# Performance work log

Hardware: AMD Instinct MI355X
Metric: run time of the kernel (lower is better)

The kernel has to match this reference:

```python
import jax, jax.numpy as jnp
import numpy as np

D_MODEL = 1024
NHEAD = 16
D_K = D_MODEL // NHEAD


def setup_inputs() -> dict:
    key = jax.random.key(0)
    ks = jax.random.split(key, 12)
    B, S = 1, 4096
    s = 1.0 / np.sqrt(D_MODEL)
    inp = {
        "query": jax.random.normal(ks[0], (B, S, D_MODEL), jnp.float32),
        "key": jax.random.normal(ks[1], (B, S, D_MODEL), jnp.float32),
        "value": jax.random.normal(ks[2], (B, S, D_MODEL), jnp.float32),
        "W_q": jax.random.normal(ks[3], (D_MODEL, D_MODEL), jnp.float32) * s,
        "b_q": jnp.zeros((D_MODEL,), jnp.float32),
        "W_k": jax.random.normal(ks[4], (D_MODEL, D_MODEL), jnp.float32) * s,
        "b_k": jnp.zeros((D_MODEL,), jnp.float32),
        "W_v": jax.random.normal(ks[5], (D_MODEL, D_MODEL), jnp.float32) * s,
        "b_v": jnp.zeros((D_MODEL,), jnp.float32),
        "W_o": jax.random.normal(ks[6], (D_MODEL, D_MODEL), jnp.float32) * s,
        "b_o": jnp.zeros((D_MODEL,), jnp.float32),
    }
    return inp


def reference(query, key, value, W_q, b_q, W_k, b_k, W_v, b_v, W_o, b_o):
    B, S, _ = query.shape
    # linear projections (torch Linear: x @ W.T + b)
    Q = query @ W_q.T + b_q
    K = key @ W_k.T + b_k
    V = value @ W_v.T + b_v
    # split heads: [B, S, D] -> [B, H, S, d_k]
    Q = Q.reshape(B, S, NHEAD, D_K).transpose(0, 2, 1, 3)
    K = K.reshape(B, S, NHEAD, D_K).transpose(0, 2, 1, 3)
    V = V.reshape(B, S, NHEAD, D_K).transpose(0, 2, 1, 3)
    # scaled dot-product attention (materializes [B,H,S,S] like original)
    scores = jnp.einsum("bhqd,bhkd->bhqk", Q, K) / jnp.sqrt(jnp.float32(D_K))
    weights = jax.nn.softmax(scores, axis=-1)
    attn = jnp.einsum("bhqk,bhkd->bhqd", weights, V)
    # combine heads: [B, H, S, d_k] -> [B, S, D]
    attn = attn.transpose(0, 2, 1, 3).reshape(B, S, D_MODEL)
    return attn @ W_o.T + b_o
```

## Files before the change

kernel.cpp:

```cpp
#include <hip/hip_runtime.h>
#include <hip/hip_bf16.h>
#include <type_traits>

constexpr int SEQ = 4096;
constexpr int DMODEL = 1024;
constexpr int NH = 16;
constexpr int DKH = 64;
constexpr float SCALE = 0.125f;
constexpr float SCALE2 = 0.125f * 1.4426950408889634f;

typedef __bf16 bf16x8 __attribute__((ext_vector_type(8)));
typedef __bf16 bf16x4 __attribute__((ext_vector_type(4)));
typedef float f32x4 __attribute__((ext_vector_type(4)));
typedef float f32x16 __attribute__((ext_vector_type(16)));
typedef unsigned int u32x4 __attribute__((ext_vector_type(4)));
union W8 { u32x4 u; bf16x8 v; };

__device__ inline void store_c(__hip_bfloat16* p, float v) { *p = __float2bfloat16(v); }
__device__ inline void store_c(float* p, float v) { *p = v; }

typedef const void __attribute__((address_space(1)))* gas_ptr;
typedef void __attribute__((address_space(3)))* las_ptr;
__device__ inline void load_lds_16B(const void* g, void* l) {
  __builtin_amdgcn_global_load_lds((gas_ptr)g, (las_ptr)l, 16, 0, 0);
}

__device__ inline unsigned pack2(float a, float b) {
  union { __bf16 h[2]; unsigned u; } p;
  p.h[0] = (__bf16)a; p.h[1] = (__bf16)b;
  return p.u;
}

__device__ inline void st8(__hip_bfloat16* buf, int row, int col, bf16x8 v) {
  *(bf16x8*)(buf + row * 64 + (col ^ ((row & 7) << 3))) = v;
}
__device__ inline bf16x8 ld8(const __hip_bfloat16* buf, int row, int col) {
  return *(const bf16x8*)(buf + row * 64 + (col ^ ((row & 7) << 3)));
}

__global__ __launch_bounds__(256)
void cvt_all(const float* __restrict__ q, const float* __restrict__ k,
             const float* __restrict__ v, const float* __restrict__ wq,
             const float* __restrict__ wk, const float* __restrict__ wv,
             const float* __restrict__ wo,
             __bf16* __restrict__ Xq, __bf16* __restrict__ Xk,
             __bf16* __restrict__ Xv, __bf16* __restrict__ Wqb,
             __bf16* __restrict__ Wkb, __bf16* __restrict__ Wvb,
             __bf16* __restrict__ Wob) {
  const int b = blockIdx.x;
  const float* src; __bf16* dst; size_t base;
  if      (b < 2048) { src = q;  dst = Xq;  base = b; }
  else if (b < 4096) { src = k;  dst = Xk;  base = b - 2048; }
  else if (b < 6144) { src = v;  dst = Xv;  base = b - 4096; }
  else if (b < 6656) { src = wq; dst = Wqb; base = b - 6144; }
  else if (b < 7168) { src = wk; dst = Wkb; base = b - 6656; }
  else if (b < 7680) { src = wv; dst = Wvb; base = b - 7168; }
  else               { src = wo; dst = Wob; base = b - 7680; }
  const size_t i = (base * 256 + threadIdx.x) * 8;
  const float4 a = *(const float4*)(src + i);
  const float4 c = *(const float4*)(src + i + 4);
  bf16x8 r = {(__bf16)a.x, (__bf16)a.y, (__bf16)a.z, (__bf16)a.w,
              (__bf16)c.x, (__bf16)c.y, (__bf16)c.z, (__bf16)c.w};
  *(bf16x8*)(dst + i) = r;
}

constexpr int BK = 64;

template <typename TC, bool TRANS_C>
__global__ __launch_bounds__(256)
void gemm_bf16_lds(const __bf16* __restrict__ A,
                   const __bf16* __restrict__ W,
                   const float* __restrict__ bias,
                   TC* __restrict__ C,
                   float out_scale) {
  __shared__ alignas(16) __bf16 As[64][64];
  __shared__ alignas(16) __bf16 Ws[64][64];

  const int t = threadIdx.x;
  const int lane = t & 63;
  const int w = t >> 6;
  const int wr = w >> 1;
  const int wc = w & 1;
  const int col = lane & 15;
  const int quad = lane >> 4;
  const int m_blk = blockIdx.y * 64;
  const int n_blk = blockIdx.x * 64;

  const int srow = t >> 3;
  const int scol = (t & 7) * 8;

  f32x4 acc[2][2] = {};

  for (int k0 = 0; k0 < DMODEL; k0 += BK) {
    __syncthreads();
    #pragma unroll
    for (int p = 0; p < 2; ++p)
      load_lds_16B(A + (size_t)(m_blk + p * 32 + srow) * DMODEL + k0 + scol,
                   &As[p * 32 + srow][scol]);
    #pragma unroll
    for (int p = 0; p < 2; ++p)
      load_lds_16B(W + (size_t)(n_blk + p * 32 + srow) * DMODEL + k0 + scol,
                   &Ws[p * 32 + srow][scol]);
    __syncthreads();

    #pragma unroll
    for (int kh = 0; kh < BK; kh += 32) {
      bf16x8 af[2], bfr[2];
      #pragma unroll
      for (int at = 0; at < 2; ++at)
        af[at] = *(const bf16x8*)&As[wr * 32 + at * 16 + col][kh + quad * 8];
      #pragma unroll
      for (int bt = 0; bt < 2; ++bt)
        bfr[bt] = *(const bf16x8*)&Ws[wc * 32 + bt * 16 + col][kh + quad * 8];
      #pragma unroll
      for (int at = 0; at < 2; ++at)
        #pragma unroll
        for (int bt = 0; bt < 2; ++bt)
          acc[at][bt] = __builtin_amdgcn_mfma_f32_16x16x32_bf16(
              af[at], bfr[bt], acc[at][bt], 0, 0, 0);
    }
  }

  #pragma unroll
  for (int at = 0; at < 2; ++at) {
    #pragma unroll
    for (int bt = 0; bt < 2; ++bt) {
      const int n = n_blk + wc * 32 + bt * 16 + col;
      const float b = bias[n];
      #pragma unroll
      for (int i = 0; i < 4; ++i) {
        const int m = m_blk + wr * 32 + at * 16 + quad * 4 + i;
        const float v = (acc[at][bt][i] + b) * out_scale;
        if constexpr (TRANS_C) store_c(&C[(size_t)n * SEQ + m], v);
        else                   store_c(&C[(size_t)m * DMODEL + n], v);
      }
    }
  }
}

constexpr int LDK = 72;

template <typename TA, typename TC, bool TRANS_C>
__global__ __launch_bounds__(256)
void gemm_tiled(const TA* __restrict__ A,
                const float* __restrict__ W,
                const float* __restrict__ bias,
                TC* __restrict__ C,
                float out_scale) {
  __shared__ alignas(16) __bf16 As[128][LDK];
  __shared__ alignas(16) __bf16 Ws[64][LDK];

  const int t = threadIdx.x;
  const int lane = t & 63;
  const int w = t >> 6;
  const int wr = w >> 1;
  const int wc = w & 1;
  const int col = lane & 15;
  const int quad = lane >> 4;
  const int m_blk = blockIdx.y * 128;
  const int n_blk = blockIdx.x * 64;

  f32x4 acc[4][2] = {};

  for (int k0 = 0; k0 < DMODEL; k0 += BK) {
    __syncthreads();
    if constexpr (std::is_same<TA, float>::value) {
      #pragma unroll
      for (int p = 0; p < 8; ++p) {
        const int r = p * 16 + (t >> 4);
        const int c = (t & 15) * 4;
        const float4 v =
            *(const float4*)(A + (size_t)(m_blk + r) * DMODEL + k0 + c);
        bf16x4 b = {(__bf16)v.x, (__bf16)v.y, (__bf16)v.z, (__bf16)v.w};
        *(bf16x4*)&As[r][c] = b;
      }
    } else {
      #pragma unroll
      for (int p = 0; p < 4; ++p) {
        const int r = p * 32 + (t >> 3);
        const int c = (t & 7) * 8;
        *(bf16x8*)&As[r][c] =
            *(const bf16x8*)((const __bf16*)A + (size_t)(m_blk + r) * DMODEL + k0 + c);
      }
    }
    #pragma unroll
    for (int p = 0; p < 4; ++p) {
      const int r = p * 16 + (t >> 4);
      const int c = (t & 15) * 4;
      const float4 v =
          *(const float4*)(W + (size_t)(n_blk + r) * DMODEL + k0 + c);
      bf16x4 b = {(__bf16)v.x, (__bf16)v.y, (__bf16)v.z, (__bf16)v.w};
      *(bf16x4*)&Ws[r][c] = b;
    }
    __syncthreads();

    #pragma unroll
    for (int kh = 0; kh < BK; kh += 32) {
      bf16x8 af[4], bfr[2];
      #pragma unroll
      for (int at = 0; at < 4; ++at)
        af[at] = *(const bf16x8*)&As[wr * 64 + at * 16 + col][kh + quad * 8];
      #pragma unroll
      for (int bt = 0; bt < 2; ++bt)
        bfr[bt] = *(const bf16x8*)&Ws[wc * 32 + bt * 16 + col][kh + quad * 8];
      #pragma unroll
      for (int at = 0; at < 4; ++at)
        #pragma unroll
        for (int bt = 0; bt < 2; ++bt)
          acc[at][bt] = __builtin_amdgcn_mfma_f32_16x16x32_bf16(
              af[at], bfr[bt], acc[at][bt], 0, 0, 0);
    }
  }

  #pragma unroll
  for (int at = 0; at < 4; ++at) {
    #pragma unroll
    for (int bt = 0; bt < 2; ++bt) {
      const int n = n_blk + wc * 32 + bt * 16 + col;
      const float b = bias[n];
      #pragma unroll
      for (int i = 0; i < 4; ++i) {
        const int m = m_blk + wr * 64 + at * 16 + quad * 4 + i;
        const float v = (acc[at][bt][i] + b) * out_scale;
        if constexpr (TRANS_C) store_c(&C[(size_t)n * SEQ + m], v);
        else                   store_c(&C[(size_t)m * DMODEL + n], v);
      }
    }
  }
}

__global__ __launch_bounds__(256, 4)
void flash_attn_split32(const __hip_bfloat16* __restrict__ Q,
                        const __hip_bfloat16* __restrict__ K,
                        const __hip_bfloat16* __restrict__ Vt,
                        __hip_bfloat16* __restrict__ Opart,
                        float* __restrict__ lsum_g) {
  __shared__ alignas(16) __hip_bfloat16 kt[64 * 64];
  __shared__ alignas(16) __hip_bfloat16 vtt[64 * 64];

  const int t = threadIdx.x;
  const int lane = t & 63;
  const int w = t >> 6;
  const int head = blockIdx.y;
  const int q0 = blockIdx.x * 128;
  const int z = blockIdx.z;
  const int l31 = lane & 31;
  const int hl = lane >> 5;

  bf16x8 qf[4];
  {
    const __hip_bfloat16* qp =
        Q + (size_t)(q0 + w * 32 + l31) * DMODEL + head * DKH + hl * 8;
    #pragma unroll
    for (int db = 0; db < 4; ++db) qf[db] = *(const bf16x8*)(qp + db * 16);
  }

  f32x16 acc_o[2] = {};
  float lsa = 0.f, lsb = 0.f;

  const int sr = t >> 2;
  const int sc = (t & 3) * 16;
  const int kbeg = z * (SEQ / 2);
  constexpr int NT = (SEQ / 2) / 64;

  const __hip_bfloat16* kgp = K + (size_t)(kbeg + sr) * DMODEL + head * DKH + sc;
  const __hip_bfloat16* vgp = Vt + (size_t)(head * DKH + sr) * SEQ + kbeg + sc;

  bf16x8 kr0 = *(const bf16x8*)kgp;
  bf16x8 kr1 = *(const bf16x8*)(kgp + 8);
  bf16x8 vr0 = *(const bf16x8*)vgp;
  bf16x8 vr1 = *(const bf16x8*)(vgp + 8);

  for (int ti = 0; ti < NT; ++ti) {
    __syncthreads();
    st8(kt, sr, sc, kr0);  st8(kt, sr, sc + 8, kr1);
    st8(vtt, sr, sc, vr0); st8(vtt, sr, sc + 8, vr1);
    __syncthreads();

    if (ti + 1 < NT) {
      const __hip_bfloat16* kn = kgp + (size_t)(ti + 1) * 64 * DMODEL;
      const __hip_bfloat16* vn = vgp + (ti + 1) * 64;
      kr0 = *(const bf16x8*)kn; kr1 = *(const bf16x8*)(kn + 8);
      vr0 = *(const bf16x8*)vn; vr1 = *(const bf16x8*)(vn + 8);
    }

    bf16x8 pa[4];
    #pragma unroll
    for (int kb = 0; kb < 2; ++kb) {
      f32x16 s = {};
      #pragma unroll
      for (int db = 0; db < 4; ++db) {
        const bf16x8 kf = ld8(kt, kb * 32 + l31, db * 16 + hl * 8);
        s = __builtin_amdgcn_mfma_f32_32x32x16_bf16(kf, qf[db], s, 0, 0, 0);
      }
      unsigned wp[8];
      #pragma unroll
      for (int i = 0; i < 8; ++i) {
        const float p0 = __builtin_amdgcn_exp2f(s[2 * i]);
        const float p1 = __builtin_amdgcn_exp2f(s[2 * i + 1]);
        lsa += p0; lsb += p1;
        wp[i] = pack2(p0, p1);
      }
      #pragma unroll
      for (int b = 0; b < 2; ++b) {
        const unsigned x0 = (unsigned)__shfl_xor((int)wp[4 * b + 0], 32);
        const unsigned x1 = (unsigned)__shfl_xor((int)wp[4 * b + 1], 32);
        const unsigned x2 = (unsigned)__shfl_xor((int)wp[4 * b + 2], 32);
        const unsigned x3 = (unsigned)__shfl_xor((int)wp[4 * b + 3], 32);
        W8 u;
        u.u[0] = hl ? x2 : wp[4 * b + 0];
        u.u[1] = hl ? x3 : wp[4 * b + 1];
        u.u[2] = hl ? wp[4 * b + 2] : x0;
        u.u[3] = hl ? wp[4 * b + 3] : x1;
        pa[kb * 2 + b] = u.v;
      }
    }

    #pragma unroll
    for (int db = 0; db < 2; ++db)
      #pragma unroll
      for (int kq = 0; kq < 4; ++kq) {
        const bf16x8 vb = ld8(vtt, db * 32 + l31, kq * 16 + hl * 8);
        acc_o[db] = __builtin_amdgcn_mfma_f32_32x32x16_bf16(
            pa[kq], vb, acc_o[db], 0, 0, 0);
      }
  }

  float lsumq = lsa + lsb;
  lsumq += __shfl_xor(lsumq, 32);
  if (lane < 32)
    lsum_g[((size_t)z * NH + head) * SEQ + q0 + w * 32 + lane] = lsumq;

  __hip_bfloat16* O = Opart + (size_t)z * SEQ * DMODEL;
  #pragma unroll
  for (int db = 0; db < 2; ++db)
    #pragma unroll
    for (int r = 0; r < 16; ++r) {
      const int qr = q0 + w * 32 + (r & 3) + 8 * (r >> 2) + 4 * hl;
      const int c = head * DKH + db * 32 + l31;
      O[(size_t)qr * DMODEL + c] = __float2bfloat16(acc_o[db][r]);
    }
}

__global__ __launch_bounds__(256)
void attn_combine(const __hip_bfloat16* __restrict__ Op,
                  const float* __restrict__ ls,
                  __hip_bfloat16* __restrict__ Ao) {
  const size_t i = ((size_t)blockIdx.x * 256 + threadIdx.x) * 8;
  const int qrow = (int)(i >> 10);
  const int h = (int)((i & 1023) >> 6);
  const float inv = 1.f / (ls[(size_t)h * SEQ + qrow] +
                           ls[(size_t)(NH + h) * SEQ + qrow]);
  const bf16x8 a = *(const bf16x8*)(Op + i);
  const bf16x8 b = *(const bf16x8*)(Op + (size_t)SEQ * DMODEL + i);
  bf16x8 r;
  #pragma unroll
  for (int j = 0; j < 8; ++j)
    r[j] = (__bf16)(((float)a[j] + (float)b[j]) * inv);
  *(bf16x8*)(Ao + i) = r;
}

constexpr int LDP = 72;
constexpr float SHIFT = 8.0f;

__global__ __launch_bounds__(256)
void flash_attn_mono(const __hip_bfloat16* __restrict__ Q,
                     const __hip_bfloat16* __restrict__ K,
                     const __hip_bfloat16* __restrict__ Vt,
                     __hip_bfloat16* __restrict__ O) {
  __shared__ alignas(16) __hip_bfloat16 kt[64][LDP];
  __shared__ alignas(16) __hip_bfloat16 vtt[DKH][LDP];
  __shared__ alignas(16) __hip_bfloat16 plT[4][32][LDP];

  const int t = threadIdx.x;
  const int lane = t & 63;
  const int w = t >> 6;
  const int h = blockIdx.y;
  const int q0 = blockIdx.x * 128;
  const int col = lane & 15;
  const int quad = lane >> 4;

  bf16x8 qf[2][2];
  #pragma unroll
  for (int rg = 0; rg < 2; ++rg) {
    const __hip_bfloat16* qptr =
        Q + (size_t)(q0 + w * 32 + rg * 16 + col) * DMODEL + h * DKH + quad * 8;
    qf[rg][0] = *(const bf16x8*)qptr;
    qf[rg][1] = *(const bf16x8*)(qptr + 32);
  }

  f32x4 acc_o[2][4] = {};
  float lsumq[2] = {0.f, 0.f};
  const int sr = t >> 2;
  const int sc = (t & 3) * 16;

  for (int k0 = 0; k0 < SEQ; k0 += 64) {
    __syncthreads();
    const __hip_bfloat16* kg = K + (size_t)(k0 + sr) * DMODEL + h * DKH + sc;
    *(bf16x8*)&kt[sr][sc]     = *(const bf16x8*)kg;
    *(bf16x8*)&kt[sr][sc + 8] = *(const bf16x8*)(kg + 8);
    const __hip_bfloat16* vg = Vt + (size_t)(h * DKH + sr) * SEQ + k0 + sc;
    *(bf16x8*)&vtt[sr][sc]     = *(const bf16x8*)vg;
    *(bf16x8*)&vtt[sr][sc + 8] = *(const bf16x8*)(vg + 8);
    __syncthreads();

    #pragma unroll
    for (int jt = 0; jt < 4; ++jt) {
      const bf16x8 kf0 = *(const bf16x8*)&kt[jt * 16 + col][quad * 8];
      const bf16x8 kf1 = *(const bf16x8*)&kt[jt * 16 + col][quad * 8 + 32];
      #pragma unroll
      for (int rg = 0; rg < 2; ++rg) {
        f32x4 zz = {0.f, 0.f, 0.f, 0.f};
        zz = __builtin_amdgcn_mfma_f32_16x16x32_bf16(kf0, qf[rg][0], zz, 0, 0, 0);
        zz = __builtin_amdgcn_mfma_f32_16x16x32_bf16(kf1, qf[rg][1], zz, 0, 0, 0);
        bf16x4 pk;
        #pragma unroll
        for (int r = 0; r < 4; ++r) {
          const float p = __expf(zz[r] - SHIFT);
          lsumq[rg] += p;
          pk[r] = (__bf16)p;
        }
        *(bf16x4*)&plT[w][rg * 16 + col][jt * 16 + quad * 4] = pk;
      }
    }

    bf16x8 pa[2][2];
    #pragma unroll
    for (int rg = 0; rg < 2; ++rg) {
      pa[rg][0] = *(const bf16x8*)&plT[w][rg * 16 + col][quad * 8];
      pa[rg][1] = *(const bf16x8*)&plT[w][rg * 16 + col][quad * 8 + 32];
    }
    #pragma unroll
    for (int jt = 0; jt < 4; ++jt) {
      const bf16x8 vb0 = *(const bf16x8*)&vtt[jt * 16 + col][quad * 8];
      const bf16x8 vb1 = *(const bf16x8*)&vtt[jt * 16 + col][quad * 8 + 32];
      #pragma unroll
      for (int rg = 0; rg < 2; ++rg) {
        acc_o[rg][jt] = __builtin_amdgcn_mfma_f32_16x16x32_bf16(
            pa[rg][0], vb0, acc_o[rg][jt], 0, 0, 0);
        acc_o[rg][jt] = __builtin_amdgcn_mfma_f32_16x16x32_bf16(
            pa[rg][1], vb1, acc_o[rg][jt], 0, 0, 0);
      }
    }
  }

  #pragma unroll
  for (int rg = 0; rg < 2; ++rg) {
    lsumq[rg] += __shfl_xor(lsumq[rg], 16);
    lsumq[rg] += __shfl_xor(lsumq[rg], 32);
  }
  float invr[2][4];
  #pragma unroll
  for (int rg = 0; rg < 2; ++rg)
    #pragma unroll
    for (int r = 0; r < 4; ++r)
      invr[rg][r] = 1.f / __shfl(lsumq[rg], quad * 4 + r);

  #pragma unroll
  for (int rg = 0; rg < 2; ++rg) {
    #pragma unroll
    for (int jt = 0; jt < 4; ++jt) {
      #pragma unroll
      for (int r = 0; r < 4; ++r) {
        const int qr = q0 + w * 32 + rg * 16 + quad * 4 + r;
        const int c = h * DKH + jt * 16 + col;
        O[(size_t)qr * DMODEL + c] = __float2bfloat16(acc_o[rg][jt][r] * invr[rg][r]);
      }
    }
  }
}

extern "C" void kernel_launch(void* const* d_in, const int* in_sizes, int n_in,
                              void* d_out, int out_size, void* d_ws, size_t ws_size,
                              hipStream_t stream) {
  const float* query = (const float*)d_in[0];
  const float* key   = (const float*)d_in[1];
  const float* value = (const float*)d_in[2];
  const float* W_q   = (const float*)d_in[3];
  const float* b_q   = (const float*)d_in[4];
  const float* W_k   = (const float*)d_in[5];
  const float* b_k   = (const float*)d_in[6];
  const float* W_v   = (const float*)d_in[7];
  const float* b_v   = (const float*)d_in[8];
  const float* W_o   = (const float*)d_in[9];
  const float* b_o   = (const float*)d_in[10];

  float* out = (float*)d_out;
  const size_t mat = (size_t)SEQ * DMODEL;
  const size_t MB = 1024 * 1024;

  char* ws = (char*)d_ws;
  __hip_bfloat16* Qp = (__hip_bfloat16*)d_out;
  __hip_bfloat16* Kp = (__hip_bfloat16*)ws;
  __hip_bfloat16* Vt = Kp + mat;

  dim3 gblock(256);
  dim3 ggrid(DMODEL / 64, SEQ / 64);

  if (ws_size >= 40 * MB) {
    __bf16* Xq  = (__bf16*)((char*)d_out + 8 * MB);
    __bf16* Xk  = (__bf16*)(ws + 16 * MB);
    __bf16* Xv  = (__bf16*)(ws + 24 * MB);
    __bf16* Wqb = (__bf16*)(ws + 32 * MB);
    __bf16* Wkb = (__bf16*)(ws + 34 * MB);
    __bf16* Wvb = (__bf16*)(ws + 36 * MB);
    __bf16* Wob = (__bf16*)(ws + 38 * MB);
    __hip_bfloat16* Opart = (__hip_bfloat16*)(ws + 16 * MB);
    float* lsum = (float*)(ws + 32 * MB);
    __hip_bfloat16* Ao = (__hip_bfloat16*)(ws + 16 * MB);

    hipLaunchKernelGGL(cvt_all, dim3(8192), gblock, 0, stream,
                       query, key, value, W_q, W_k, W_v, W_o,
                       Xq, Xk, Xv, Wqb, Wkb, Wvb, Wob);

    hipLaunchKernelGGL((gemm_bf16_lds<__hip_bfloat16, false>), ggrid, gblock,
                       0, stream, Xq, Wqb, b_q, Qp, SCALE2);
    hipLaunchKernelGGL((gemm_bf16_lds<__hip_bfloat16, false>), ggrid, gblock,
                       0, stream, Xk, Wkb, b_k, Kp, 1.0f);
    hipLaunchKernelGGL((gemm_bf16_lds<__hip_bfloat16, true>), ggrid, gblock,
                       0, stream, Xv, Wvb, b_v, Vt, 1.0f);

    dim3 agrid(SEQ / 128, NH, 2);
    hipLaunchKernelGGL(flash_attn_split32, agrid, gblock, 0, stream,
                       Qp, Kp, Vt, Opart, lsum);
    hipLaunchKernelGGL(attn_combine, dim3(2048), gblock, 0, stream,
                       Opart, lsum, Ao);

    hipLaunchKernelGGL((gemm_bf16_lds<float, false>), ggrid, gblock, 0, stream,
                       (const __bf16*)Ao, Wob, b_o, out, 1.0f);
  } else {
    __hip_bfloat16* Ao = Qp + mat;
    float* Cw = (float*)d_ws;
    dim3 fgrid(DMODEL / 64, SEQ / 128);
    hipLaunchKernelGGL((gemm_tiled<float, __hip_bfloat16, false>), fgrid, gblock,
                       0, stream, query, W_q, b_q, Qp, SCALE);
    hipLaunchKernelGGL((gemm_tiled<float, __hip_bfloat16, false>), fgrid, gblock,
                       0, stream, key, W_k, b_k, Kp, 1.0f);
    hipLaunchKernelGGL((gemm_tiled<float, __hip_bfloat16, true>), fgrid, gblock,
                       0, stream, value, W_v, b_v, Vt, 1.0f);
    dim3 agrid(SEQ / 128, NH);
    hipLaunchKernelGGL(flash_attn_mono, agrid, gblock, 0, stream, Qp, Kp, Vt, Ao);
    hipLaunchKernelGGL((gemm_tiled<__hip_bfloat16, float, false>), fgrid, gblock,
                       0, stream, Ao, W_o, b_o, Cw, 1.0f);
    hipMemcpyAsync(out, Cw, mat * sizeof(float), hipMemcpyDeviceToDevice, stream);
  }
}
```

Measured before the change: 293.6 us.

## Double-buffer LDS tiles in GEMM and flash attention, use permlane32 swap

Both the projection GEMM and the split flash-attention kernel now keep two LDS buffers. The next tile is written while the current one is consumed, so each iteration needs one barrier instead of two and global latency overlaps with MFMA work. The attention kernel also replaces its xor-32 shuffles and selects with v_permlane32_swap. It raises wave priority around MFMA blocks and splits the PV accumulator in two to shorten the dependency chain. The cost is twice the LDS footprint and more registers, which could limit occupancy.

Measured after the change: 412.7 us. 40.6% more time.

```diff
diff --git a/kernel.cpp b/kernel.cpp
--- a/kernel.cpp
+++ b/kernel.cpp
@@ -73,8 +73,8 @@
                    const float* __restrict__ bias,
                    TC* __restrict__ C,
                    float out_scale) {
-  __shared__ alignas(16) __bf16 As[64][64];
-  __shared__ alignas(16) __bf16 Ws[64][64];
+  __shared__ alignas(16) __bf16 As[2][64][64];
+  __shared__ alignas(16) __bf16 Ws[2][64][64];
 
   const int t = threadIdx.x;
   const int lane = t & 63;
@@ -91,27 +91,39 @@
 
   f32x4 acc[2][2] = {};
 
+  const __bf16* Ab = A + (size_t)(m_blk + srow) * DMODEL + scol;
+  const __bf16* Wb = W + (size_t)(n_blk + srow) * DMODEL + scol;
+
+  #pragma unroll
+  for (int p = 0; p < 2; ++p)
+    load_lds_16B(Ab + (size_t)p * 32 * DMODEL, &As[0][p * 32 + srow][scol]);
+  #pragma unroll
+  for (int p = 0; p < 2; ++p)
+    load_lds_16B(Wb + (size_t)p * 32 * DMODEL, &Ws[0][p * 32 + srow][scol]);
+  __syncthreads();
+
+  int cur = 0;
   for (int k0 = 0; k0 < DMODEL; k0 += BK) {
-    __syncthreads();
-    #pragma unroll
-    for (int p = 0; p < 2; ++p)
-      load_lds_16B(A + (size_t)(m_blk + p * 32 + srow) * DMODEL + k0 + scol,
-                   &As[p * 32 + srow][scol]);
-    #pragma unroll
-    for (int p = 0; p < 2; ++p)
-      load_lds_16B(W + (size_t)(n_blk + p * 32 + srow) * DMODEL + k0 + scol,
-                   &Ws[p * 32 + srow][scol]);
-    __syncthreads();
+    if (k0 + BK < DMODEL) {
+      #pragma unroll
+      for (int p = 0; p < 2; ++p)
+        load_lds_16B(Ab + (size_t)p * 32 * DMODEL + k0 + BK,
+                     &As[cur ^ 1][p * 32 + srow][scol]);
+      #pragma unroll
+      for (int p = 0; p < 2; ++p)
+        load_lds_16B(Wb + (size_t)p * 32 * DMODEL + k0 + BK,
+                     &Ws[cur ^ 1][p * 32 + srow][scol]);
+    }
 
     #pragma unroll
     for (int kh = 0; kh < BK; kh += 32) {
       bf16x8 af[2], bfr[2];
       #pragma unroll
       for (int at = 0; at < 2; ++at)
-        af[at] = *(const bf16x8*)&As[wr * 32 + at * 16 + col][kh + quad * 8];
+        af[at] = *(const bf16x8*)&As[cur][wr * 32 + at * 16 + col][kh + quad * 8];
       #pragma unroll
       for (int bt = 0; bt < 2; ++bt)
-        bfr[bt] = *(const bf16x8*)&Ws[wc * 32 + bt * 16 + col][kh + quad * 8];
+        bfr[bt] = *(const bf16x8*)&Ws[cur][wc * 32 + bt * 16 + col][kh + quad * 8];
       #pragma unroll
       for (int at = 0; at < 2; ++at)
         #pragma unroll
@@ -119,6 +131,8 @@
           acc[at][bt] = __builtin_amdgcn_mfma_f32_16x16x32_bf16(
               af[at], bfr[bt], acc[at][bt], 0, 0, 0);
     }
+    __syncthreads();
+    cur ^= 1;
   }
 
   #pragma unroll
@@ -235,8 +249,8 @@
                         const __hip_bfloat16* __restrict__ Vt,
                         __hip_bfloat16* __restrict__ Opart,
                         float* __restrict__ lsum_g) {
-  __shared__ alignas(16) __hip_bfloat16 kt[64 * 64];
-  __shared__ alignas(16) __hip_bfloat16 vtt[64 * 64];
+  __shared__ alignas(16) __hip_bfloat16 kt[2][64 * 64];
+  __shared__ alignas(16) __hip_bfloat16 vtt[2][64 * 64];
 
   const int t = threadIdx.x;
   const int lane = t & 63;
@@ -255,7 +269,7 @@
     for (int db = 0; db < 4; ++db) qf[db] = *(const bf16x8*)(qp + db * 16);
   }
 
-  f32x16 acc_o[2] = {};
+  f32x16 acc_o[2][2] = {};
   float lsa = 0.f, lsb = 0.f;
 
   const int sr = t >> 2;
@@ -270,29 +284,43 @@
   bf16x8 kr1 = *(const bf16x8*)(kgp + 8);
   bf16x8 vr0 = *(const bf16x8*)vgp;
   bf16x8 vr1 = *(const bf16x8*)(vgp + 8);
+  st8(kt[0], sr, sc, kr0);  st8(kt[0], sr, sc + 8, kr1);
+  st8(vtt[0], sr, sc, vr0); st8(vtt[0], sr, sc + 8, vr1);
+  kr0 = *(const bf16x8*)(kgp + (size_t)64 * DMODEL);
+  kr1 = *(const bf16x8*)(kgp + (size_t)64 * DMODEL + 8);
+  vr0 = *(const bf16x8*)(vgp + 64);
+  vr1 = *(const bf16x8*)(vgp + 64 + 8);
+  __syncthreads();
 
   for (int ti = 0; ti < NT; ++ti) {
-    __syncthreads();
-    st8(kt, sr, sc, kr0);  st8(kt, sr, sc + 8, kr1);
-    st8(vtt, sr, sc, vr0); st8(vtt, sr, sc + 8, vr1);
-    __syncthreads();
+    const int cur = ti & 1;
+    const __hip_bfloat16* ktc = kt[cur];
+    const __hip_bfloat16* vtc = vtt[cur];
 
     if (ti + 1 < NT) {
-      const __hip_bfloat16* kn = kgp + (size_t)(ti + 1) * 64 * DMODEL;
-      const __hip_bfloat16* vn = vgp + (ti + 1) * 64;
-      kr0 = *(const bf16x8*)kn; kr1 = *(const bf16x8*)(kn + 8);
-      vr0 = *(const bf16x8*)vn; vr1 = *(const bf16x8*)(vn + 8);
+      __hip_bfloat16* kn = kt[cur ^ 1];
+      __hip_bfloat16* vn = vtt[cur ^ 1];
+      st8(kn, sr, sc, kr0);  st8(kn, sr, sc + 8, kr1);
+      st8(vn, sr, sc, vr0);  st8(vn, sr, sc + 8, vr1);
+      if (ti + 2 < NT) {
+        const __hip_bfloat16* kg = kgp + (size_t)(ti + 2) * 64 * DMODEL;
+        const __hip_bfloat16* vg = vgp + (ti + 2) * 64;
+        kr0 = *(const bf16x8*)kg; kr1 = *(const bf16x8*)(kg + 8);
+        vr0 = *(const bf16x8*)vg; vr1 = *(const bf16x8*)(vg + 8);
+      }
     }
 
     bf16x8 pa[4];
     #pragma unroll
     for (int kb = 0; kb < 2; ++kb) {
       f32x16 s = {};
+      __builtin_amdgcn_s_setprio(1);
       #pragma unroll
       for (int db = 0; db < 4; ++db) {
-        const bf16x8 kf = ld8(kt, kb * 32 + l31, db * 16 + hl * 8);
+        const bf16x8 kf = ld8(ktc, kb * 32 + l31, db * 16 + hl * 8);
         s = __builtin_amdgcn_mfma_f32_32x32x16_bf16(kf, qf[db], s, 0, 0, 0);
       }
+      __builtin_amdgcn_s_setprio(0);
       unsigned wp[8];
       #pragma unroll
       for (int i = 0; i < 8; ++i) {
@@ -303,27 +331,28 @@
       }
       #pragma unroll
       for (int b = 0; b < 2; ++b) {
-        const unsigned x0 = (unsigned)__shfl_xor((int)wp[4 * b + 0], 32);
-        const unsigned x1 = (unsigned)__shfl_xor((int)wp[4 * b + 1], 32);
-        const unsigned x2 = (unsigned)__shfl_xor((int)wp[4 * b + 2], 32);
-        const unsigned x3 = (unsigned)__shfl_xor((int)wp[4 * b + 3], 32);
+        unsigned a0 = wp[4 * b + 0], a2 = wp[4 * b + 2];
+        unsigned a1 = wp[4 * b + 1], a3 = wp[4 * b + 3];
+        asm("v_permlane32_swap_b32 %0, %1" : "+v"(a0), "+v"(a2));
+        asm("v_permlane32_swap_b32 %0, %1" : "+v"(a1), "+v"(a3));
         W8 u;
-        u.u[0] = hl ? x2 : wp[4 * b + 0];
-        u.u[1] = hl ? x3 : wp[4 * b + 1];
-        u.u[2] = hl ? wp[4 * b + 2] : x0;
-        u.u[3] = hl ? wp[4 * b + 3] : x1;
+        u.u[0] = a0; u.u[1] = a1; u.u[2] = a2; u.u[3] = a3;
         pa[kb * 2 + b] = u.v;
       }
     }
 
+    __builtin_amdgcn_s_setprio(1);
     #pragma unroll
     for (int db = 0; db < 2; ++db)
       #pragma unroll
       for (int kq = 0; kq < 4; ++kq) {
-        const bf16x8 vb = ld8(vtt, db * 32 + l31, kq * 16 + hl * 8);
-        acc_o[db] = __builtin_amdgcn_mfma_f32_32x32x16_bf16(
-            pa[kq], vb, acc_o[db], 0, 0, 0);
-      }
+        const bf16x8 vb = ld8(vtc, db * 32 + l31, kq * 16 + hl * 8);
+        acc_o[db][kq & 1] = __builtin_amdgcn_mfma_f32_32x32x16_bf16(
+            pa[kq], vb, acc_o[db][kq & 1], 0, 0, 0);
+      }
+    __builtin_amdgcn_s_setprio(0);
+
+    __syncthreads();
   }
 
   float lsumq = lsa + lsb;
@@ -333,13 +362,15 @@
 
   __hip_bfloat16* O = Opart + (size_t)z * SEQ * DMODEL;
   #pragma unroll
-  for (int db = 0; db < 2; ++db)
+  for (int db = 0; db < 2; ++db) {
+    const f32x16 af = acc_o[db][0] + acc_o[db][1];
     #pragma unroll
     for (int r = 0; r < 16; ++r) {
       const int qr = q0 + w * 32 + (r & 3) + 8 * (r >> 2) + 4 * hl;
       const int c = head * DKH + db * 32 + l31;
-      O[(size_t)qr * DMODEL + c] = __float2bfloat16(acc_o[db][r]);
-    }
+      O[(size_t)qr * DMODEL + c] = __float2bfloat16(af[r]);
+    }
+  }
 }
 
 __global__ __launch_bounds__(256)
```
